# Performance work log

Measured on AMD Instinct MI355X. Metric: run time of the kernel, lower is better.

Reference implementation:

```python
import math
import jax, jax.numpy as jnp
import numpy as np

D_MODEL = 768
N_HEADS = 12
D_K = 64
D_V = 64
LN_EPS = 1e-5


def setup_inputs() -> dict:
    key = jax.random.key(0)
    ks = jax.random.split(key, 12)
    B, S = 4, 2048
    Q = jax.random.normal(ks[0], (B, S, D_MODEL), dtype=jnp.float32)
    K = jax.random.normal(ks[1], (B, S, D_MODEL), dtype=jnp.float32)
    V = jax.random.normal(ks[2], (B, S, D_MODEL), dtype=jnp.float32)
    attn_mask = jax.random.randint(ks[3], (B, S, S), 0, 2).astype(bool)
    sc = 1.0 / math.sqrt(D_MODEL)
    WQ = jax.random.normal(ks[4], (D_MODEL, N_HEADS * D_K), dtype=jnp.float32) * sc
    WK = jax.random.normal(ks[5], (D_MODEL, N_HEADS * D_K), dtype=jnp.float32) * sc
    WV = jax.random.normal(ks[6], (D_MODEL, N_HEADS * D_V), dtype=jnp.float32) * sc
    Wfc = jax.random.normal(ks[7], (N_HEADS * D_V, D_MODEL), dtype=jnp.float32) * sc
    bQ = jnp.zeros((N_HEADS * D_K,), jnp.float32)
    bK = jnp.zeros((N_HEADS * D_K,), jnp.float32)
    bV = jnp.zeros((N_HEADS * D_V,), jnp.float32)
    bfc = jnp.zeros((D_MODEL,), jnp.float32)
    gamma = jnp.ones((D_MODEL,), jnp.float32)
    beta = jnp.zeros((D_MODEL,), jnp.float32)
    return {"Q": Q, "K": K, "V": V, "attn_mask": attn_mask,
            "WQ": WQ, "bQ": bQ, "WK": WK, "bK": bK, "WV": WV, "bV": bV,
            "Wfc": Wfc, "bfc": bfc, "gamma": gamma, "beta": beta}


def reference(Q, K, V, attn_mask, WQ, bQ, WK, bK, WV, bV, Wfc, bfc, gamma, beta):
    B, S, _ = Q.shape
    # projections -> [B, H, S, d]
    q = (Q @ WQ + bQ).reshape(B, S, N_HEADS, D_K).transpose(0, 2, 1, 3)
    k = (K @ WK + bK).reshape(B, S, N_HEADS, D_K).transpose(0, 2, 1, 3)
    v = (V @ WV + bV).reshape(B, S, N_HEADS, D_V).transpose(0, 2, 1, 3)
    # manual scaled dot-product attention with masked_fill(-1e9)
    scores = jnp.einsum('bhqd,bhkd->bhqk', q, k) / math.sqrt(D_K)
    scores = jnp.where(attn_mask[:, None, :, :], jnp.float32(-1e9), scores)
    attn = jax.nn.softmax(scores, axis=-1)
    context = jnp.einsum('bhqk,bhkd->bhqd', attn, v)
    context = context.transpose(0, 2, 1, 3).reshape(B, S, N_HEADS * D_V)
    out = context @ Wfc + bfc + Q  # residual is Q
    # LayerNorm over d_model
    mu = jnp.mean(out, axis=-1, keepdims=True)
    var = jnp.mean((out - mu) ** 2, axis=-1, keepdims=True)
    return (out - mu) * jax.lax.rsqrt(var + LN_EPS) * gamma + beta
```

## Files before the change

kernel.cpp:

```cpp
#include <hip/hip_runtime.h>
#include <stdint.h>

#define DM   768
#define HEADS 12
#define DK    64
#define SEQ  2048
#define BATCH  4

typedef __bf16 bf16_t;
typedef __bf16 bf16x8 __attribute__((ext_vector_type(8)));
typedef __bf16 bf16x4 __attribute__((ext_vector_type(4)));
typedef float  f32x4  __attribute__((ext_vector_type(4)));
typedef float  f32x16 __attribute__((ext_vector_type(16)));
typedef unsigned u32x4 __attribute__((ext_vector_type(4)));

#define LOG2E 1.44269504f
#define MASKVAL (-1.442695e9f)
#define DEFER_THR 8.0f

#define OFF_FLAG 0
#define OFF_MASK 256
#define SZ_MASK  (BATCH*SEQ*(SEQ/32)*4)
#define OFF_WT   (OFF_MASK + SZ_MASK)
#define SZ_WT1   (DM*DM*2)
#define OFF_XB   (OFF_WT + 4*SZ_WT1)
#define SZ_X     (BATCH*SEQ*DM*2)
#define OFF_QP   (OFF_XB + 3*SZ_X)
#define SZ_PROJ  (BATCH*HEADS*SEQ*DK*2)
#define OFF_KP   (OFF_QP + SZ_PROJ)
#define OFF_VT   (OFF_KP + SZ_PROJ)
#define OFF_ML   (OFF_VT + SZ_PROJ)
#define SZ_ML    (2*BATCH*HEADS*SEQ*2*4)

__device__ __forceinline__ void gload_lds16(const bf16_t* g, bf16_t* l) {
    __builtin_amdgcn_global_load_lds((const __attribute__((address_space(1))) unsigned int*)g,
                                     (__attribute__((address_space(3))) unsigned int*)l, 16, 0, 0);
}

__device__ __forceinline__ unsigned pack2(float lo, float hi) {
    union { bf16_t b[2]; unsigned u; } x;
    x.b[0] = (bf16_t)lo; x.b[1] = (bf16_t)hi;
    return x.u;
}

__global__ void detect_mask_kernel(const unsigned char* __restrict__ m, int* flag) {
    int u = threadIdx.x;
    int any = m[4*u+1] | m[4*u+2] | m[4*u+3];
    unsigned long long b = __ballot(any != 0);
    if (u == 0) *flag = (b == 0ULL) ? 1 : 0;
}

__global__ void pack_mask_kernel(const void* __restrict__ mraw, const int* __restrict__ flag,
                                 unsigned int* __restrict__ words) {
    const unsigned int total = BATCH*SEQ*SEQ;
    const int is32 = *flag;
    const int* mi = (const int*)mraw;
    const unsigned char* mb = (const unsigned char*)mraw;
    unsigned int stride = gridDim.x * blockDim.x;
    unsigned int lane = threadIdx.x & 63u;
    for (unsigned int e = blockIdx.x * blockDim.x + threadIdx.x; e < total; e += stride) {
        int v = is32 ? (mi[e] != 0) : (mb[e] != 0);
        unsigned long long bal = __ballot(v);
        if ((lane & 31u) == 0u)
            words[e >> 5] = (unsigned int)(bal >> ((lane >> 5) * 32u));
    }
}

__global__ void wt_cvt_kernel(const float* __restrict__ W0, const float* __restrict__ W1,
                              const float* __restrict__ W2, const float* __restrict__ W3,
                              bf16_t* __restrict__ dst) {
    const float* W = blockIdx.z == 0 ? W0 : blockIdx.z == 1 ? W1 : blockIdx.z == 2 ? W2 : W3;
    bf16_t* out = dst + (size_t)blockIdx.z * DM * DM;
    __shared__ float tile[64][65];
    int w = threadIdx.x >> 6, u = threadIdx.x & 63;
    int kb = blockIdx.x * 64, nb = blockIdx.y * 64;
    #pragma unroll
    for (int i = 0; i < 16; i++)
        tile[w + 4*i][u] = W[(size_t)(kb + w + 4*i)*DM + nb + u];
    __syncthreads();
    #pragma unroll
    for (int i = 0; i < 16; i++)
        out[(size_t)(nb + w + 4*i)*DM + kb + u] = (bf16_t)tile[u][w + 4*i];
}

__global__ void xcvt_kernel(const float* __restrict__ Q, const float* __restrict__ K,
                            const float* __restrict__ V, bf16_t* __restrict__ XB) {
    int z = blockIdx.y;
    const float* src = z == 0 ? Q : z == 1 ? K : V;
    bf16_t* dst = XB + (size_t)z * BATCH*SEQ*DM;
    size_t i = ((size_t)blockIdx.x * blockDim.x + threadIdx.x) * 8;
    float4 a = *(const float4*)(src + i);
    float4 b = *(const float4*)(src + i + 4);
    bf16x8 o;
    o[0]=(bf16_t)a.x; o[1]=(bf16_t)a.y; o[2]=(bf16_t)a.z; o[3]=(bf16_t)a.w;
    o[4]=(bf16_t)b.x; o[5]=(bf16_t)b.y; o[6]=(bf16_t)b.z; o[7]=(bf16_t)b.w;
    *(bf16x8*)(dst + i) = o;
}

__device__ __forceinline__ void mm_mainloop256(const bf16_t* __restrict__ Aptr,
                                               const bf16_t* __restrict__ Bptr,
                                               bf16_t* As, bf16_t* Bs,
                                               f32x4 acc[4][6], int bm, int bn) {
    int tid = threadIdx.x, w = tid >> 6, u = tid & 63, c = u & 15, g = u >> 4;
    for (int k0 = 0; k0 < DM; k0 += 64) {
        #pragma unroll
        for (int i = 0; i < 8; i++) {
            int q = i*256 + tid;
            int row = q >> 3, col8 = q & 7;
            gload_lds16(Aptr + (size_t)(bm*256 + row)*DM + k0 + col8*8, As + (i*256 + w*64)*8);
        }
        #pragma unroll
        for (int i = 0; i < 3; i++) {
            int q = i*256 + tid;
            int row = q >> 3, col8 = q & 7;
            gload_lds16(Bptr + (size_t)(bn*96 + row)*DM + k0 + col8*8, Bs + (i*256 + w*64)*8);
        }
        __syncthreads();
        #pragma unroll
        for (int kk = 0; kk < 2; kk++) {
            bf16x8 a[4], bfr[6];
            #pragma unroll
            for (int mi = 0; mi < 4; mi++)
                a[mi] = *(const bf16x8*)(As + (w*64 + mi*16 + c)*64 + kk*32 + g*8);
            #pragma unroll
            for (int ni = 0; ni < 6; ni++)
                bfr[ni] = *(const bf16x8*)(Bs + (ni*16 + c)*64 + kk*32 + g*8);
            #pragma unroll
            for (int mi = 0; mi < 4; mi++)
                #pragma unroll
                for (int ni = 0; ni < 6; ni++)
                    acc[mi][ni] = __builtin_amdgcn_mfma_f32_16x16x32_bf16(a[mi], bfr[ni], acc[mi][ni], 0, 0, 0);
        }
        __syncthreads();
    }
}

__global__ __launch_bounds__(256) void proj256_kernel(
        const bf16_t* __restrict__ XB, const bf16_t* __restrict__ WT,
        const float* __restrict__ bQ, const float* __restrict__ bK, const float* __restrict__ bV,
        bf16_t* __restrict__ QP, bf16_t* __restrict__ KP, bf16_t* __restrict__ VT) {
    int z = blockIdx.z;
    const bf16_t* Aptr = XB + (size_t)z * BATCH*SEQ*DM;
    const bf16_t* Bptr = WT + (size_t)z * DM * DM;
    const float* bias = z == 0 ? bQ : z == 1 ? bK : bV;
    float scale = (z == 0) ? 0.125f * LOG2E : 1.0f;
    __shared__ __align__(16) bf16_t As[256*64], Bs[96*64];
    int tid = threadIdx.x, w = tid >> 6, u = tid & 63, c = u & 15, g = u >> 4;
    int bm = blockIdx.x, bn = blockIdx.y;
    f32x4 zero = {0.f,0.f,0.f,0.f};
    f32x4 acc[4][6] = {{zero,zero,zero,zero,zero,zero},{zero,zero,zero,zero,zero,zero},
                       {zero,zero,zero,zero,zero,zero},{zero,zero,zero,zero,zero,zero}};
    mm_mainloop256(Aptr, Bptr, As, Bs, acc, bm, bn);
    #pragma unroll
    for (int ni = 0; ni < 6; ni++) {
        int n = bn*96 + ni*16 + c;
        int h = n >> 6, d = n & 63;
        float bv = bias[n];
        if (z < 2) {
            bf16_t* dst = (z == 0) ? QP : KP;
            #pragma unroll
            for (int mi = 0; mi < 4; mi++)
                #pragma unroll
                for (int j = 0; j < 4; j++) {
                    int r = bm*256 + w*64 + mi*16 + 4*g + j;
                    int bidx = r >> 11, s = r & 2047;
                    dst[(((size_t)bidx*HEADS + h)*SEQ + s)*DK + d] = (bf16_t)((acc[mi][ni][j] + bv)*scale);
                }
        } else {
            #pragma unroll
            for (int mi = 0; mi < 4; mi++) {
                bf16x4 pk;
                #pragma unroll
                for (int j = 0; j < 4; j++) pk[j] = (bf16_t)(acc[mi][ni][j] + bv);
                int r0 = bm*256 + w*64 + mi*16 + 4*g;
                int bidx = r0 >> 11, s0 = r0 & 2047;
                *(bf16x4*)(VT + (((size_t)bidx*HEADS + h)*DK + d)*SEQ + s0) = pk;
            }
        }
    }
}

__global__ __launch_bounds__(256) void out256_kernel(
        const bf16_t* __restrict__ CTX, const bf16_t* __restrict__ WfcT,
        const float* __restrict__ bfc, const float* __restrict__ Qres, float* __restrict__ out) {
    __shared__ __align__(16) bf16_t As[256*64], Bs[96*64];
    int tid = threadIdx.x, w = tid >> 6, u = tid & 63, c = u & 15, g = u >> 4;
    int bm = blockIdx.x, bn = blockIdx.y;
    f32x4 zero = {0.f,0.f,0.f,0.f};
    f32x4 acc[4][6] = {{zero,zero,zero,zero,zero,zero},{zero,zero,zero,zero,zero,zero},
                       {zero,zero,zero,zero,zero,zero},{zero,zero,zero,zero,zero,zero}};
    mm_mainloop256(CTX, WfcT, As, Bs, acc, bm, bn);
    #pragma unroll
    for (int ni = 0; ni < 6; ni++) {
        int n = bn*96 + ni*16 + c;
        float bv = bfc[n];
        #pragma unroll
        for (int mi = 0; mi < 4; mi++)
            #pragma unroll
            for (int j = 0; j < 4; j++) {
                int r = bm*256 + w*64 + mi*16 + 4*g + j;
                out[(size_t)r*DM + n] = acc[mi][ni][j] + bv + Qres[(size_t)r*DM + n];
            }
    }
}

__global__ __launch_bounds__(256) void attn_kernel(
        const bf16_t* __restrict__ QP, const bf16_t* __restrict__ KP, const bf16_t* __restrict__ VT,
        const unsigned int* __restrict__ maskw, bf16_t* __restrict__ OP, float* __restrict__ ML) {
    __shared__ __align__(16) bf16_t kbuf[2][64*64];
    __shared__ __align__(16) bf16_t vbuf[2][64*64];
    __shared__ __align__(16) float lut4[64];
    int tid = threadIdx.x, w = tid >> 6, u = tid & 63;
    int qc = u & 31, hi = u >> 5;
    int sp = blockIdx.z & 1, b = blockIdx.z >> 1, h = blockIdx.y;
    int kvbase = sp << 10;
    int qg = blockIdx.x * 128 + w * 32 + qc;
    size_t bh = (size_t)(b * HEADS + h);
    const bf16_t* qp = QP + bh * SEQ * DK;
    const bf16_t* kp = KP + bh * SEQ * DK;
    const bf16_t* vt = VT + bh * DK * SEQ;
    const unsigned int* mwq = maskw + ((size_t)b * SEQ + qg) * (SEQ/32);

    if (tid < 64) lut4[tid] = (((tid >> 2) >> (tid & 3)) & 1) ? MASKVAL : 0.f;

    bf16x8 qf[4];
    #pragma unroll
    for (int t = 0; t < 4; t++)
        qf[t] = *(const bf16x8*)(qp + (size_t)qg*DK + 16*t + 8*hi);

    int sr = tid >> 3, scc = tid & 7;

    f32x16 zz = {0,0,0,0,0,0,0,0,0,0,0,0,0,0,0,0};
    f32x16 acc0 = zz, acc1 = zz;
    float mrun = -16384.0f, lsum = 0.f;

    #pragma unroll
    for (int i = 0; i < 2; i++) {
        int r = i*32 + sr;
        int gc = (scc ^ (r & 7)) << 3;
        gload_lds16(kp + (size_t)(kvbase + r)*DK + gc,   &kbuf[0][0] + i*2048 + tid*8);
        gload_lds16(vt + (size_t)r*SEQ + kvbase + gc,    &vbuf[0][0] + i*2048 + tid*8);
    }
    uint2 mv = *(const uint2*)(mwq + (kvbase >> 5));
    __syncthreads();

    for (int kt = 0; kt < 16; kt++) {
        int kb = kvbase + kt * 64;
        int cur = kt & 1;
        uint2 mv_next = mv;
        if (kt + 1 < 16) {
            mv_next = *(const uint2*)(mwq + ((kb + 64) >> 5));
            int nkb = kb + 64;
            #pragma unroll
            for (int i = 0; i < 2; i++) {
                int r = i*32 + sr;
                int gc = (scc ^ (r & 7)) << 3;
                gload_lds16(kp + (size_t)(nkb + r)*DK + gc, &kbuf[cur^1][0] + i*2048 + tid*8);
                gload_lds16(vt + (size_t)r*SEQ + nkb + gc,  &vbuf[cur^1][0] + i*2048 + tid*8);
            }
        }
        const bf16_t* kl = &kbuf[cur][0];
        const bf16_t* vl = &vbuf[cur][0];

        f32x4 am0[4], am1[4];
        #pragma unroll
        for (int j = 0; j < 4; j++) {
            am0[j] = *(const f32x4*)&lut4[((mv.x >> (8*j + 4*hi)) & 0xFu) * 4];
            am1[j] = *(const f32x4*)&lut4[((mv.y >> (8*j + 4*hi)) & 0xFu) * 4];
        }

        f32x16 s0 = zz, s1 = zz;
        __builtin_amdgcn_s_setprio(1);
        #pragma unroll
        for (int t = 0; t < 4; t++) {
            int col = (16*t + 8*hi);
            int r0 = qc, r1 = 32 + qc;
            bf16x8 k0 = *(const bf16x8*)(kl + r0*64 + (col ^ ((r0 & 7) << 3)));
            bf16x8 k1 = *(const bf16x8*)(kl + r1*64 + (col ^ ((r1 & 7) << 3)));
            s0 = __builtin_amdgcn_mfma_f32_32x32x16_bf16(k0, qf[t], s0, 0, 0, 0);
            s1 = __builtin_amdgcn_mfma_f32_32x32x16_bf16(k1, qf[t], s1, 0, 0, 0);
        }
        __builtin_amdgcn_s_setprio(0);

        #pragma unroll
        for (int j = 0; j < 4; j++)
            #pragma unroll
            for (int i = 0; i < 4; i++) {
                s0[4*j + i] += am0[j][i];
                s1[4*j + i] += am1[j][i];
            }

        float q8[8];
        #pragma unroll
        for (int r = 0; r < 8; r++)
            q8[r] = fmaxf(fmaxf(s0[r], s0[r+8]), fmaxf(s1[r], s1[r+8]));
        float q4a = fmaxf(fmaxf(q8[0], q8[1]), fmaxf(q8[2], q8[3]));
        float q4b = fmaxf(fmaxf(q8[4], q8[5]), fmaxf(q8[6], q8[7]));
        float tm = fmaxf(q4a, q4b);

        if (!__all(tm <= mrun + DEFER_THR)) {
            float rmax = fmaxf(tm, __shfl_xor(tm, 32));
            float mn = fmaxf(mrun, rmax);
            float alpha = __builtin_amdgcn_exp2f(mrun - mn);
            mrun = mn;
            lsum *= alpha;
            acc0 *= alpha;
            acc1 *= alpha;
        }

        #pragma unroll
        for (int r = 0; r < 16; r++) {
            s0[r] = __builtin_amdgcn_exp2f(s0[r] - mrun);
            s1[r] = __builtin_amdgcn_exp2f(s1[r] - mrun);
        }
        f32x16 sv = s0 + s1;
        float a8[8];
        #pragma unroll
        for (int r = 0; r < 8; r++) a8[r] = sv[r] + sv[r+8];
        float a4a = (a8[0] + a8[1]) + (a8[2] + a8[3]);
        float a4b = (a8[4] + a8[5]) + (a8[6] + a8[7]);
        float rsum = a4a + a4b;
        lsum += rsum + __shfl_xor(rsum, 32);

        bf16x8 pa[4];
        {
            union { u32x4 uv; bf16x8 bv; } cv;
            unsigned x0, y0, x1, y1;
            x0 = pack2(s0[0], s0[1]); y0 = pack2(s0[4], s0[5]);
            asm volatile("v_permlane32_swap_b32 %0, %1" : "+v"(x0), "+v"(y0));
            x1 = pack2(s0[2], s0[3]); y1 = pack2(s0[6], s0[7]);
            asm volatile("v_permlane32_swap_b32 %0, %1" : "+v"(x1), "+v"(y1));
            cv.uv[0]=x0; cv.uv[1]=x1; cv.uv[2]=y0; cv.uv[3]=y1; pa[0]=cv.bv;
            x0 = pack2(s0[8], s0[9]);  y0 = pack2(s0[12], s0[13]);
            asm volatile("v_permlane32_swap_b32 %0, %1" : "+v"(x0), "+v"(y0));
            x1 = pack2(s0[10], s0[11]); y1 = pack2(s0[14], s0[15]);
            asm volatile("v_permlane32_swap_b32 %0, %1" : "+v"(x1), "+v"(y1));
            cv.uv[0]=x0; cv.uv[1]=x1; cv.uv[2]=y0; cv.uv[3]=y1; pa[1]=cv.bv;
            x0 = pack2(s1[0], s1[1]); y0 = pack2(s1[4], s1[5]);
            asm volatile("v_permlane32_swap_b32 %0, %1" : "+v"(x0), "+v"(y0));
            x1 = pack2(s1[2], s1[3]); y1 = pack2(s1[6], s1[7]);
            asm volatile("v_permlane32_swap_b32 %0, %1" : "+v"(x1), "+v"(y1));
            cv.uv[0]=x0; cv.uv[1]=x1; cv.uv[2]=y0; cv.uv[3]=y1; pa[2]=cv.bv;
            x0 = pack2(s1[8], s1[9]);  y0 = pack2(s1[12], s1[13]);
            asm volatile("v_permlane32_swap_b32 %0, %1" : "+v"(x0), "+v"(y0));
            x1 = pack2(s1[10], s1[11]); y1 = pack2(s1[14], s1[15]);
            asm volatile("v_permlane32_swap_b32 %0, %1" : "+v"(x1), "+v"(y1));
            cv.uv[0]=x0; cv.uv[1]=x1; cv.uv[2]=y0; cv.uv[3]=y1; pa[3]=cv.bv;
        }

        __builtin_amdgcn_s_setprio(1);
        #pragma unroll
        for (int ks = 0; ks < 4; ks++) {
            int col = 16*ks + 8*hi;
            int r0 = qc, r1 = 32 + qc;
            bf16x8 v0 = *(const bf16x8*)(vl + r0*64 + (col ^ ((r0 & 7) << 3)));
            bf16x8 v1 = *(const bf16x8*)(vl + r1*64 + (col ^ ((r1 & 7) << 3)));
            acc0 = __builtin_amdgcn_mfma_f32_32x32x16_bf16(v0, pa[ks], acc0, 0, 0, 0);
            acc1 = __builtin_amdgcn_mfma_f32_32x32x16_bf16(v1, pa[ks], acc1, 0, 0, 0);
        }
        __builtin_amdgcn_s_setprio(0);

        __syncthreads();
        mv = mv_next;
    }

    size_t prow = ((size_t)(sp * BATCH + b) * HEADS + h) * SEQ + qg;
    #pragma unroll
    for (int gr = 0; gr < 4; gr++) {
        bf16x4 o0, o1;
        #pragma unroll
        for (int jj = 0; jj < 4; jj++) {
            o0[jj] = (bf16_t)acc0[4*gr + jj];
            o1[jj] = (bf16_t)acc1[4*gr + jj];
        }
        *(bf16x4*)(OP + prow*DK + gr*8 + hi*4)      = o0;
        *(bf16x4*)(OP + prow*DK + 32 + gr*8 + hi*4) = o1;
    }
    if (hi == 0) {
        float2 ml = {mrun, lsum};
        *(float2*)(ML + prow*2) = ml;
    }
}

__global__ __launch_bounds__(256) void attn_combine_kernel(
        const bf16_t* __restrict__ OP, const float* __restrict__ ML, bf16_t* __restrict__ CTX) {
    int tid = threadIdx.x;
    int r = tid >> 2, dc = (tid & 3) << 4;
    int h = blockIdx.y, b = blockIdx.z;
    int q = blockIdx.x * 64 + r;
    const size_t P = (size_t)BATCH * HEADS * SEQ;
    size_t row0 = ((size_t)b * HEADS + h) * SEQ + q;
    size_t row1 = row0 + P;
    float2 ml0 = *(const float2*)(ML + row0*2);
    float2 ml1 = *(const float2*)(ML + row1*2);
    float M = fmaxf(ml0.x, ml1.x);
    float w0 = exp2f(ml0.x - M), w1 = exp2f(ml1.x - M);
    float inv = 1.0f / (w0*ml0.y + w1*ml1.y);
    w0 *= inv; w1 *= inv;
    const bf16x8* pa = (const bf16x8*)(OP + row0*DK + dc);
    const bf16x8* pb = (const bf16x8*)(OP + row1*DK + dc);
    bf16_t* dst = CTX + ((size_t)b*SEQ + q)*DM + h*DK + dc;
    #pragma unroll
    for (int k = 0; k < 2; k++) {
        bf16x8 av = pa[k], bv = pb[k];
        bf16x8 o;
        #pragma unroll
        for (int i = 0; i < 8; i++)
            o[i] = (bf16_t)((float)av[i]*w0 + (float)bv[i]*w1);
        *(bf16x8*)(dst + k*8) = o;
    }
}

__global__ __launch_bounds__(256) void ln_kernel(float* __restrict__ out,
        const float* __restrict__ gamma, const float* __restrict__ beta) {
    int w = threadIdx.x >> 6, u = threadIdx.x & 63;
    size_t row = (size_t)blockIdx.x * 4 + w;
    float x[12];
    float s = 0.f;
    #pragma unroll
    for (int i = 0; i < 12; i++) { x[i] = out[row*DM + i*64 + u]; s += x[i]; }
    #pragma unroll
    for (int d = 1; d < 64; d <<= 1) s += __shfl_xor(s, d);
    float mu = s * (1.0f/768.0f);
    float v = 0.f;
    #pragma unroll
    for (int i = 0; i < 12; i++) { float t = x[i] - mu; v += t*t; }
    #pragma unroll
    for (int d = 1; d < 64; d <<= 1) v += __shfl_xor(v, d);
    float rstd = rsqrtf(v * (1.0f/768.0f) + 1e-5f);
    #pragma unroll
    for (int i = 0; i < 12; i++)
        out[row*DM + i*64 + u] = (x[i] - mu) * rstd * gamma[i*64 + u] + beta[i*64 + u];
}

extern "C" void kernel_launch(void* const* d_in, const int* in_sizes, int n_in,
                              void* d_out, int out_size, void* d_ws, size_t ws_size,
                              hipStream_t stream) {
    const float* Q    = (const float*)d_in[0];
    const float* K    = (const float*)d_in[1];
    const float* V    = (const float*)d_in[2];
    const void*  mask = d_in[3];
    const float* WQ   = (const float*)d_in[4];
    const float* bQ   = (const float*)d_in[5];
    const float* WK   = (const float*)d_in[6];
    const float* bK   = (const float*)d_in[7];
    const float* WV   = (const float*)d_in[8];
    const float* bV   = (const float*)d_in[9];
    const float* Wfc  = (const float*)d_in[10];
    const float* bfc  = (const float*)d_in[11];
    const float* gam  = (const float*)d_in[12];
    const float* bet  = (const float*)d_in[13];
    float* out = (float*)d_out;
    char* ws = (char*)d_ws;

    int* flag            = (int*)(ws + OFF_FLAG);
    unsigned int* maskw  = (unsigned int*)(ws + OFF_MASK);
    bf16_t* WT           = (bf16_t*)(ws + OFF_WT);
    bf16_t* XB           = (bf16_t*)(ws + OFF_XB);
    bf16_t* QP           = (bf16_t*)(ws + OFF_QP);
    bf16_t* KP           = (bf16_t*)(ws + OFF_KP);
    bf16_t* VT           = (bf16_t*)(ws + OFF_VT);
    float*  ML           = (float*)(ws + OFF_ML);
    bf16_t* CTX          = XB;
    bf16_t* OP           = (bf16_t*)(ws + OFF_XB + SZ_X);

    detect_mask_kernel<<<1, 64, 0, stream>>>((const unsigned char*)mask, flag);
    pack_mask_kernel<<<2048, 256, 0, stream>>>(mask, flag, maskw);
    xcvt_kernel<<<dim3(3072, 3), 256, 0, stream>>>(Q, K, V, XB);
    wt_cvt_kernel<<<dim3(12, 12, 4), 256, 0, stream>>>(WQ, WK, WV, Wfc, WT);
    proj256_kernel<<<dim3(32, 8, 3), 256, 0, stream>>>(XB, WT, bQ, bK, bV, QP, KP, VT);
    attn_kernel<<<dim3(SEQ/128, HEADS, BATCH*2), 256, 0, stream>>>(QP, KP, VT, maskw, OP, ML);
    attn_combine_kernel<<<dim3(SEQ/64, HEADS, BATCH), 256, 0, stream>>>(OP, ML, CTX);
    out256_kernel<<<dim3(32, 8), 256, 0, stream>>>(CTX, WT + (size_t)3*DM*DM, bfc, Q, out);
    ln_kernel<<<2048, 256, 0, stream>>>(out, gam, bet);
}
```

Baseline: 396.3 us.

## Retile projection GEMMs to 128x192 with swizzled grid and staged VT stores

The projection and output GEMMs move from 256x96 tiles to 128x192 tiles on a 2x2 wave layout, with a grouped block-index mapping meant to improve L2 reuse. The V-transpose output is now staged through LDS so it can be written as 16-byte vector stores. The separate mask-detection kernel is folded into pack_mask, which removes one launch. In attention, the mask bias is loaded straight into the MFMA accumulator instead of being added afterwards. The extra LDS staging adds barriers, and each block now reads the first mask words redundantly.

```diff
diff --git a/kernel.cpp b/kernel.cpp
--- a/kernel.cpp
+++ b/kernel.cpp
@@ -43,17 +43,12 @@
     return x.u;
 }
 
-__global__ void detect_mask_kernel(const unsigned char* __restrict__ m, int* flag) {
-    int u = threadIdx.x;
-    int any = m[4*u+1] | m[4*u+2] | m[4*u+3];
-    unsigned long long b = __ballot(any != 0);
-    if (u == 0) *flag = (b == 0ULL) ? 1 : 0;
-}
-
-__global__ void pack_mask_kernel(const void* __restrict__ mraw, const int* __restrict__ flag,
+__global__ void pack_mask_kernel(const unsigned int* __restrict__ mraw,
                                  unsigned int* __restrict__ words) {
+    int is32 = 1;
+    #pragma unroll
+    for (int i = 0; i < 64; i++) is32 &= ((mraw[i] & 0xFFFFFF00u) == 0u);
     const unsigned int total = BATCH*SEQ*SEQ;
-    const int is32 = *flag;
     const int* mi = (const int*)mraw;
     const unsigned char* mb = (const unsigned char*)mraw;
     unsigned int stride = gridDim.x * blockDim.x;
@@ -97,23 +92,26 @@
     *(bf16x8*)(dst + i) = o;
 }
 
-__device__ __forceinline__ void mm_mainloop256(const bf16_t* __restrict__ Aptr,
+__device__ __forceinline__ void mm_mainloop192(const bf16_t* __restrict__ Aptr,
                                                const bf16_t* __restrict__ Bptr,
-                                               bf16_t* As, bf16_t* Bs,
+                                               bf16_t* smem,
                                                f32x4 acc[4][6], int bm, int bn) {
-    int tid = threadIdx.x, w = tid >> 6, u = tid & 63, c = u & 15, g = u >> 4;
+    bf16_t* As = smem;
+    bf16_t* Bs = smem + 128*64;
+    int tid = threadIdx.x, u = tid & 63, c = u & 15, g = u >> 4;
+    int w = tid >> 6, wr = w & 1, wc = w >> 1;
     for (int k0 = 0; k0 < DM; k0 += 64) {
         #pragma unroll
-        for (int i = 0; i < 8; i++) {
+        for (int i = 0; i < 4; i++) {
             int q = i*256 + tid;
             int row = q >> 3, col8 = q & 7;
-            gload_lds16(Aptr + (size_t)(bm*256 + row)*DM + k0 + col8*8, As + (i*256 + w*64)*8);
-        }
-        #pragma unroll
-        for (int i = 0; i < 3; i++) {
+            gload_lds16(Aptr + (size_t)(bm*128 + row)*DM + k0 + col8*8, As + q*8);
+        }
+        #pragma unroll
+        for (int i = 0; i < 6; i++) {
             int q = i*256 + tid;
             int row = q >> 3, col8 = q & 7;
-            gload_lds16(Bptr + (size_t)(bn*96 + row)*DM + k0 + col8*8, Bs + (i*256 + w*64)*8);
+            gload_lds16(Bptr + (size_t)(bn*192 + row)*DM + k0 + col8*8, Bs + q*8);
         }
         __syncthreads();
         #pragma unroll
@@ -121,10 +119,10 @@
             bf16x8 a[4], bfr[6];
             #pragma unroll
             for (int mi = 0; mi < 4; mi++)
-                a[mi] = *(const bf16x8*)(As + (w*64 + mi*16 + c)*64 + kk*32 + g*8);
+                a[mi] = *(const bf16x8*)(As + (wr*64 + mi*16 + c)*64 + kk*32 + g*8);
             #pragma unroll
             for (int ni = 0; ni < 6; ni++)
-                bfr[ni] = *(const bf16x8*)(Bs + (ni*16 + c)*64 + kk*32 + g*8);
+                bfr[ni] = *(const bf16x8*)(Bs + (wc*96 + ni*16 + c)*64 + kk*32 + g*8);
             #pragma unroll
             for (int mi = 0; mi < 4; mi++)
                 #pragma unroll
@@ -135,70 +133,98 @@
     }
 }
 
-__global__ __launch_bounds__(256) void proj256_kernel(
+__device__ __forceinline__ void grid_map(int lin, int& bm, int& bn) {
+    bm = ((lin >> 5) << 3) | (lin & 7);
+    bn = (lin >> 3) & 3;
+}
+
+__global__ __launch_bounds__(256) void proj192_kernel(
         const bf16_t* __restrict__ XB, const bf16_t* __restrict__ WT,
         const float* __restrict__ bQ, const float* __restrict__ bK, const float* __restrict__ bV,
         bf16_t* __restrict__ QP, bf16_t* __restrict__ KP, bf16_t* __restrict__ VT) {
-    int z = blockIdx.z;
+    int z = blockIdx.y;
     const bf16_t* Aptr = XB + (size_t)z * BATCH*SEQ*DM;
     const bf16_t* Bptr = WT + (size_t)z * DM * DM;
     const float* bias = z == 0 ? bQ : z == 1 ? bK : bV;
     float scale = (z == 0) ? 0.125f * LOG2E : 1.0f;
-    __shared__ __align__(16) bf16_t As[256*64], Bs[96*64];
-    int tid = threadIdx.x, w = tid >> 6, u = tid & 63, c = u & 15, g = u >> 4;
-    int bm = blockIdx.x, bn = blockIdx.y;
+    __shared__ __align__(16) bf16_t smem[128*64 + 192*64];
+    int tid = threadIdx.x, u = tid & 63, c = u & 15, g = u >> 4;
+    int w = tid >> 6, wr = w & 1, wc = w >> 1;
+    int bm, bn; grid_map(blockIdx.x, bm, bn);
     f32x4 zero = {0.f,0.f,0.f,0.f};
     f32x4 acc[4][6] = {{zero,zero,zero,zero,zero,zero},{zero,zero,zero,zero,zero,zero},
                        {zero,zero,zero,zero,zero,zero},{zero,zero,zero,zero,zero,zero}};
-    mm_mainloop256(Aptr, Bptr, As, Bs, acc, bm, bn);
-    #pragma unroll
-    for (int ni = 0; ni < 6; ni++) {
-        int n = bn*96 + ni*16 + c;
-        int h = n >> 6, d = n & 63;
-        float bv = bias[n];
-        if (z < 2) {
-            bf16_t* dst = (z == 0) ? QP : KP;
+    mm_mainloop192(Aptr, Bptr, smem, acc, bm, bn);
+    if (z < 2) {
+        bf16_t* dst = (z == 0) ? QP : KP;
+        #pragma unroll
+        for (int ni = 0; ni < 6; ni++) {
+            int n = bn*192 + wc*96 + ni*16 + c;
+            int h = n >> 6, d = n & 63;
+            float bv = bias[n];
             #pragma unroll
             for (int mi = 0; mi < 4; mi++)
                 #pragma unroll
                 for (int j = 0; j < 4; j++) {
-                    int r = bm*256 + w*64 + mi*16 + 4*g + j;
+                    int r = bm*128 + wr*64 + mi*16 + 4*g + j;
                     int bidx = r >> 11, s = r & 2047;
                     dst[(((size_t)bidx*HEADS + h)*SEQ + s)*DK + d] = (bf16_t)((acc[mi][ni][j] + bv)*scale);
                 }
-        } else {
-            #pragma unroll
-            for (int mi = 0; mi < 4; mi++) {
-                bf16x4 pk;
+        }
+    } else {
+        #pragma unroll
+        for (int p = 0; p < 2; p++) {
+            if (wc == p) {
                 #pragma unroll
-                for (int j = 0; j < 4; j++) pk[j] = (bf16_t)(acc[mi][ni][j] + bv);
-                int r0 = bm*256 + w*64 + mi*16 + 4*g;
+                for (int ni = 0; ni < 6; ni++) {
+                    int n = bn*192 + wc*96 + ni*16 + c;
+                    float bv = bias[n];
+                    #pragma unroll
+                    for (int mi = 0; mi < 4; mi++)
+                        #pragma unroll
+                        for (int j = 0; j < 4; j++) {
+                            int r_loc = wr*64 + mi*16 + 4*g + j;
+                            smem[(ni*16 + c)*136 + r_loc] = (bf16_t)(acc[mi][ni][j] + bv);
+                        }
+                }
+            }
+            __syncthreads();
+            #pragma unroll
+            for (int it = 0; it < 6; it++) {
+                int idx = it*256 + tid;
+                int n_l = idx >> 4, r8 = (idx & 15) << 3;
+                bf16x8 v = *(const bf16x8*)(smem + n_l*136 + r8);
+                int n = bn*192 + p*96 + n_l;
+                int h = n >> 6, d = n & 63;
+                int r0 = bm*128 + r8;
                 int bidx = r0 >> 11, s0 = r0 & 2047;
-                *(bf16x4*)(VT + (((size_t)bidx*HEADS + h)*DK + d)*SEQ + s0) = pk;
+                *(bf16x8*)(VT + (((size_t)bidx*HEADS + h)*DK + d)*SEQ + s0) = v;
             }
-        }
-    }
-}
-
-__global__ __launch_bounds__(256) void out256_kernel(
+            __syncthreads();
+        }
+    }
+}
+
+__global__ __launch_bounds__(256) void out192_kernel(
         const bf16_t* __restrict__ CTX, const bf16_t* __restrict__ WfcT,
         const float* __restrict__ bfc, const float* __restrict__ Qres, float* __restrict__ out) {
-    __shared__ __align__(16) bf16_t As[256*64], Bs[96*64];
-    int tid = threadIdx.x, w = tid >> 6, u = tid & 63, c = u & 15, g = u >> 4;
-    int bm = blockIdx.x, bn = blockIdx.y;
+    __shared__ __align__(16) bf16_t smem[128*64 + 192*64];
+    int tid = threadIdx.x, u = tid & 63, c = u & 15, g = u >> 4;
+    int w = tid >> 6, wr = w & 1, wc = w >> 1;
+    int bm, bn; grid_map(blockIdx.x, bm, bn);
     f32x4 zero = {0.f,0.f,0.f,0.f};
     f32x4 acc[4][6] = {{zero,zero,zero,zero,zero,zero},{zero,zero,zero,zero,zero,zero},
                        {zero,zero,zero,zero,zero,zero},{zero,zero,zero,zero,zero,zero}};
-    mm_mainloop256(CTX, WfcT, As, Bs, acc, bm, bn);
+    mm_mainloop192(CTX, WfcT, smem, acc, bm, bn);
     #pragma unroll
     for (int ni = 0; ni < 6; ni++) {
-        int n = bn*96 + ni*16 + c;
+        int n = bn*192 + wc*96 + ni*16 + c;
         float bv = bfc[n];
         #pragma unroll
         for (int mi = 0; mi < 4; mi++)
             #pragma unroll
             for (int j = 0; j < 4; j++) {
-                int r = bm*256 + w*64 + mi*16 + 4*g + j;
+                int r = bm*128 + wr*64 + mi*16 + 4*g + j;
                 out[(size_t)r*DM + n] = acc[mi][ni][j] + bv + Qres[(size_t)r*DM + n];
             }
     }
@@ -262,14 +288,15 @@
         const bf16_t* kl = &kbuf[cur][0];
         const bf16_t* vl = &vbuf[cur][0];
 
-        f32x4 am0[4], am1[4];
+        f32x16 s0, s1;
         #pragma unroll
         for (int j = 0; j < 4; j++) {
-            am0[j] = *(const f32x4*)&lut4[((mv.x >> (8*j + 4*hi)) & 0xFu) * 4];
-            am1[j] = *(const f32x4*)&lut4[((mv.y >> (8*j + 4*hi)) & 0xFu) * 4];
-        }
-
-        f32x16 s0 = zz, s1 = zz;
+            f32x4 a0 = *(const f32x4*)&lut4[((mv.x >> (8*j + 4*hi)) & 0xFu) * 4];
+            f32x4 a1 = *(const f32x4*)&lut4[((mv.y >> (8*j + 4*hi)) & 0xFu) * 4];
+            #pragma unroll
+            for (int i = 0; i < 4; i++) { s0[4*j + i] = a0[i]; s1[4*j + i] = a1[i]; }
+        }
+
         __builtin_amdgcn_s_setprio(1);
         #pragma unroll
         for (int t = 0; t < 4; t++) {
@@ -281,14 +308,6 @@
             s1 = __builtin_amdgcn_mfma_f32_32x32x16_bf16(k1, qf[t], s1, 0, 0, 0);
         }
         __builtin_amdgcn_s_setprio(0);
-
-        #pragma unroll
-        for (int j = 0; j < 4; j++)
-            #pragma unroll
-            for (int i = 0; i < 4; i++) {
-                s0[4*j + i] += am0[j][i];
-                s1[4*j + i] += am1[j][i];
-            }
 
         float q8[8];
         #pragma unroll
@@ -453,7 +472,6 @@
     float* out = (float*)d_out;
     char* ws = (char*)d_ws;
 
-    int* flag            = (int*)(ws + OFF_FLAG);
     unsigned int* maskw  = (unsigned int*)(ws + OFF_MASK);
     bf16_t* WT           = (bf16_t*)(ws + OFF_WT);
     bf16_t* XB           = (bf16_t*)(ws + OFF_XB);
@@ -464,13 +482,12 @@
     bf16_t* CTX          = XB;
     bf16_t* OP           = (bf16_t*)(ws + OFF_XB + SZ_X);
 
-    detect_mask_kernel<<<1, 64, 0, stream>>>((const unsigned char*)mask, flag);
-    pack_mask_kernel<<<2048, 256, 0, stream>>>(mask, flag, maskw);
+    pack_mask_kernel<<<2048, 256, 0, stream>>>((const unsigned int*)mask, maskw);
     xcvt_kernel<<<dim3(3072, 3), 256, 0, stream>>>(Q, K, V, XB);
     wt_cvt_kernel<<<dim3(12, 12, 4), 256, 0, stream>>>(WQ, WK, WV, Wfc, WT);
-    proj256_kernel<<<dim3(32, 8, 3), 256, 0, stream>>>(XB, WT, bQ, bK, bV, QP, KP, VT);
+    proj192_kernel<<<dim3(256, 3), 256, 0, stream>>>(XB, WT, bQ, bK, bV, QP, KP, VT);
     attn_kernel<<<dim3(SEQ/128, HEADS, BATCH*2), 256, 0, stream>>>(QP, KP, VT, maskw, OP, ML);
     attn_combine_kernel<<<dim3(SEQ/64, HEADS, BATCH), 256, 0, stream>>>(OP, ML, CTX);
-    out256_kernel<<<dim3(32, 8), 256, 0, stream>>>(CTX, WT + (size_t)3*DM*DM, bfc, Q, out);
+    out192_kernel<<<256, 256, 0, stream>>>(CTX, WT + (size_t)3*DM*DM, bfc, Q, out);
     ln_kernel<<<2048, 256, 0, stream>>>(out, gam, bet);
 }
```

After: 407.7 us. 2.9% more time.
